# Performance work log

Hardware: AMD Instinct MI355X
Metric: run time of the kernel (lower is better)

Reference implementation:

```python
import jax, jax.numpy as jnp
import numpy as np

D_MODEL, N_HEADS, D_FF = 512, 8, 2048
B, L = 2, 2048


def layer_norm(x, g, b, eps=1e-5):
    mu = jnp.mean(x, axis=-1, keepdims=True)
    var = jnp.mean(jnp.square(x - mu), axis=-1, keepdims=True)
    return (x - mu) * jax.lax.rsqrt(var + eps) * g + b


def setup_inputs() -> dict:
    key = jax.random.key(0)
    ks = jax.random.split(key, 16)
    s = 1.0 / np.sqrt(D_MODEL)
    sf = 1.0 / np.sqrt(D_FF)
    return {
        "x": jax.random.normal(ks[0], (B, L, D_MODEL), jnp.float32),
        "Wq": jax.random.normal(ks[1], (D_MODEL, D_MODEL), jnp.float32) * s,
        "bq": jnp.zeros((D_MODEL,), jnp.float32),
        "Wk": jax.random.normal(ks[2], (D_MODEL, D_MODEL), jnp.float32) * s,
        "bk": jnp.zeros((D_MODEL,), jnp.float32),
        "Wv": jax.random.normal(ks[3], (D_MODEL, D_MODEL), jnp.float32) * s,
        "bv": jnp.zeros((D_MODEL,), jnp.float32),
        "Wo": jax.random.normal(ks[4], (D_MODEL, D_MODEL), jnp.float32) * s,
        "bo": jnp.zeros((D_MODEL,), jnp.float32),
        "W1": jax.random.normal(ks[5], (D_FF, D_MODEL), jnp.float32) * s,   # conv1 k=1 -> linear
        "b1": jnp.zeros((D_FF,), jnp.float32),
        "W2": jax.random.normal(ks[6], (D_MODEL, D_FF), jnp.float32) * sf,  # conv2 k=1 -> linear
        "b2": jnp.zeros((D_MODEL,), jnp.float32),
        "g1": jnp.ones((D_MODEL,), jnp.float32),
        "be1": jnp.zeros((D_MODEL,), jnp.float32),
        "g2": jnp.ones((D_MODEL,), jnp.float32),
        "be2": jnp.zeros((D_MODEL,), jnp.float32),
    }


def reference(x, Wq, bq, Wk, bk, Wv, bv, Wo, bo, W1, b1, W2, b2, g1, be1, g2, be2):
    Bx, Lx, D = x.shape
    H = N_HEADS
    dk = D // H
    # projections -> [B, L, H, dk]
    q = (x @ Wq.T + bq).reshape(Bx, Lx, H, dk)
    k = (x @ Wk.T + bk).reshape(Bx, Lx, H, dk)
    v = (x @ Wv.T + bv).reshape(Bx, Lx, H, dk)
    scale = 1.0 / jnp.sqrt(jnp.asarray(dk, x.dtype))
    scores = jnp.einsum('blhd,bshd->bhls', q, k)  # full LxL score tensor (as in source)
    A = jax.nn.softmax(scale * scores, axis=-1)
    out = jnp.einsum('bhls,bshd->blhd', A, v).reshape(Bx, Lx, D)
    attn_out = out @ Wo.T + bo
    # residual + norm1 (dropout is identity in eval)
    x1 = layer_norm(x + attn_out, g1, be1)
    # FFN: conv1d with kernel_size=1 == pointwise linear
    y = jax.nn.relu(x1 @ W1.T + b1)
    y = y @ W2.T + b2
    return layer_norm(x1 + y, g2, be2)
```

## Files before the change

### kernel.cpp

```cpp
#include <hip/hip_runtime.h>
#include <hip/hip_bf16.h>
#include <cstddef>

#define SEQ 2048
#define DM  512
#define NH  8
#define DKH 64
#define DFF 2048
#define NB  2
#define MR  (NB*SEQ)

typedef __attribute__((ext_vector_type(8)))  short short8;
typedef __attribute__((ext_vector_type(4)))  float f32x4;
typedef __attribute__((ext_vector_type(16))) float f32x16;

#define AS1(p) ((const __attribute__((address_space(1))) void*)(p))
#define AS3(p) ((__attribute__((address_space(3))) void*)(p))

#define QSCALE 0.180336880f

__device__ inline unsigned cvtpk(float lo, float hi) {
  unsigned r;
  asm("v_cvt_pk_bf16_f32 %0, %1, %2" : "=v"(r) : "v"(lo), "v"(hi));
  return r;
}

__device__ inline void cvt8(const float* __restrict__ s, __hip_bfloat16* __restrict__ d) {
  float4 a = *reinterpret_cast<const float4*>(s);
  float4 b = *reinterpret_cast<const float4*>(s + 4);
  union { __hip_bfloat16 h[8]; short8 v; } u;
  u.h[0] = __float2bfloat16(a.x); u.h[1] = __float2bfloat16(a.y);
  u.h[2] = __float2bfloat16(a.z); u.h[3] = __float2bfloat16(a.w);
  u.h[4] = __float2bfloat16(b.x); u.h[5] = __float2bfloat16(b.y);
  u.h[6] = __float2bfloat16(b.z); u.h[7] = __float2bfloat16(b.w);
  *reinterpret_cast<short8*>(d) = u.v;
}

__global__ __launch_bounds__(256) void cvt_all(
    const float* __restrict__ x,
    const float* __restrict__ Wq, const float* __restrict__ Wk,
    const float* __restrict__ Wv, const float* __restrict__ Wo,
    const float* __restrict__ W1, const float* __restrict__ W2,
    const float* __restrict__ bq, const float* __restrict__ bk,
    const float* __restrict__ bv,
    __hip_bfloat16* __restrict__ xb,  __hip_bfloat16* __restrict__ wqkv,
    __hip_bfloat16* __restrict__ wob, __hip_bfloat16* __restrict__ w1b,
    __hip_bfloat16* __restrict__ w2b, float* __restrict__ bqkv)
{
  const int u = blockIdx.x * 256 + threadIdx.x;
  if (u < 262144) {
    cvt8(x + (size_t)u * 8, xb + (size_t)u * 8);
  } else if (u < 360448) {
    const int d = (u - 262144) * 8;
    const int n = d >> 9, k = d & 511;
    const float* src = (n < 512) ? (Wq + (size_t)n * 512 + k)
                     : (n < 1024) ? (Wk + (size_t)(n - 512) * 512 + k)
                                  : (Wv + (size_t)(n - 1024) * 512 + k);
    cvt8(src, wqkv + d);
  } else if (u < 393216) {
    const int d = (u - 360448) * 8; cvt8(Wo + d, wob + d);
  } else if (u < 524288) {
    const int d = (u - 393216) * 8; cvt8(W1 + d, w1b + d);
  } else if (u < 655360) {
    const int d = (u - 524288) * 8; cvt8(W2 + d, w2b + d);
  } else if (u < 655552) {
    const int d = (u - 655360) * 8;
    const float* src = (d < 512) ? (bq + d) : (d < 1024) ? (bk + d - 512) : (bv + d - 1024);
    *reinterpret_cast<float4*>(bqkv + d)     = *reinterpret_cast<const float4*>(src);
    *reinterpret_cast<float4*>(bqkv + d + 4) = *reinterpret_cast<const float4*>(src + 4);
  }
}

template<int OUT_BF16, int RELU, int WVT, int SPLITK>
__global__ __launch_bounds__(256) void gemm_bt(
    const __hip_bfloat16* __restrict__ A, const __hip_bfloat16* __restrict__ Bt,
    const float* __restrict__ bias, void* __restrict__ Cout, void* __restrict__ Cout1,
    __hip_bfloat16* __restrict__ qkbO, __hip_bfloat16* __restrict__ vtO,
    int M, int N, int K)
{
  __shared__ __align__(16) char lds[32768];
  const int t = threadIdx.x, lane = t & 63, w = t >> 6;
  const int m0 = blockIdx.y * 128, n0 = blockIdx.x * 128;
  const int wm = w >> 1, wn = w & 1;
  const int z = (SPLITK == 2) ? blockIdx.z : 0;
  const int Keff = (SPLITK == 2) ? (K >> 1) : K;
  const int koff = z * Keff;
  const int g = lane >> 4;

  const int r0   = t >> 2;
  const int kofs = ((lane & 3) ^ (r0 & 3)) * 8;
  const __hip_bfloat16* a0 = A  + (size_t)(m0 + r0)      * K + koff + kofs;
  const __hip_bfloat16* a1 = A  + (size_t)(m0 + r0 + 64) * K + koff + kofs;
  const __hip_bfloat16* b0 = Bt + (size_t)(n0 + r0)      * K + koff + kofs;
  const __hip_bfloat16* b1 = Bt + (size_t)(n0 + r0 + 64) * K + koff + kofs;
  const int ldsoff = t * 16;

  const int ca = (lane >> 4) ^ (lane & 3);
  const int fA = (wm * 64 + (lane & 15)) * 64 + ca * 16;
  const int fB = (wn * 64 + (lane & 15)) * 64 + ca * 16;

  f32x4 acc[4][4] = {};
  const int nkt = Keff >> 5;

  auto STAGE = [&](int buf, int kt) {
    const size_t ko = (size_t)kt * 32;
    char* bb = lds + buf * 16384;
    __builtin_amdgcn_global_load_lds(AS1(a0 + ko), AS3(bb + ldsoff),         16, 0, 0);
    __builtin_amdgcn_global_load_lds(AS1(a1 + ko), AS3(bb + 4096  + ldsoff), 16, 0, 0);
    __builtin_amdgcn_global_load_lds(AS1(b0 + ko), AS3(bb + 8192  + ldsoff), 16, 0, 0);
    __builtin_amdgcn_global_load_lds(AS1(b1 + ko), AS3(bb + 12288 + ldsoff), 16, 0, 0);
  };

  STAGE(0, 0);
  __syncthreads();
  int cur = 0;

  for (int kt = 0; kt < nkt; ++kt) {
    STAGE(cur ^ 1, kt + 1 < nkt ? kt + 1 : kt);
    const char* Ab = lds + cur * 16384;
    const char* Bb = Ab + 8192;
    short8 af[4], bf[4];
#pragma unroll
    for (int i = 0; i < 4; ++i) af[i] = *reinterpret_cast<const short8*>(Ab + fA + i * 1024);
#pragma unroll
    for (int j = 0; j < 4; ++j) bf[j] = *reinterpret_cast<const short8*>(Bb + fB + j * 1024);
    __builtin_amdgcn_s_setprio(1);
#pragma unroll
    for (int i = 0; i < 4; ++i)
#pragma unroll
      for (int j = 0; j < 4; ++j)
        acc[i][j] = __builtin_amdgcn_mfma_f32_16x16x32_bf16(af[i], bf[j], acc[i][j], 0, 0, 0);
    __builtin_amdgcn_s_setprio(0);
    __syncthreads();
    cur ^= 1;
  }

  float bcol[4];
#pragma unroll
  for (int j = 0; j < 4; ++j)
    bcol[j] = (SPLITK == 2 && z) ? 0.f : bias[n0 + wn * 64 + j * 16 + (lane & 15)];

  if (WVT && n0 >= 1024) {
#pragma unroll
    for (int i = 0; i < 4; ++i) {
      const int r = m0 + wm * 64 + i * 16 + (g << 2);
      const int bb = r >> 11, s = r & 2047;
#pragma unroll
      for (int j = 0; j < 4; ++j) {
        const int hd = n0 + wn * 64 + j * 16 + (lane & 15) - 1024;
        union { __hip_bfloat16 h[4]; uint2 uu; } pk;
#pragma unroll
        for (int jj = 0; jj < 4; ++jj) pk.h[jj] = __float2bfloat16(acc[i][j][jj] + bcol[j]);
        *reinterpret_cast<uint2*>(vtO + ((size_t)(bb * 8 + (hd >> 6)) * 64 + (hd & 63)) * SEQ + s) = pk.uu;
      }
    }
    return;
  }

  const float qsc = (WVT && n0 < 512) ? QSCALE : 1.0f;
#pragma unroll
  for (int i = 0; i < 4; ++i) {
    const int row = m0 + wm * 64 + i * 16 + (g << 2);
#pragma unroll
    for (int j = 0; j < 4; ++j) {
      const int col = n0 + wn * 64 + j * 16 + (lane & 15);
#pragma unroll
      for (int jj = 0; jj < 4; ++jj) {
        float v = acc[i][j][jj] + bcol[j];
        if (RELU) v = fmaxf(v, 0.f);
        if (WVT)
          qkbO[(size_t)(row + jj) * 1024 + col] = __float2bfloat16(v * qsc);
        else if (OUT_BF16)
          ((__hip_bfloat16*)Cout)[(size_t)(row + jj) * N + col] = __float2bfloat16(v);
        else {
          float* dst = (float*)((SPLITK == 2 && z) ? Cout1 : Cout);
          dst[(size_t)(row + jj) * N + col] = v;
        }
      }
    }
  }
}

__global__ __launch_bounds__(256) void attn_mfma(
    const __hip_bfloat16* __restrict__ qkb, const __hip_bfloat16* __restrict__ vtb,
    __hip_bfloat16* __restrict__ po, float* __restrict__ pm, float* __restrict__ pl)
{
  __shared__ __align__(16) char lds[32768];
  char* ks = lds;
  char* vT = lds + 16384;

  const int t = threadIdx.x, lane = t & 63, w = t >> 6;
  const int qt = blockIdx.x, bh = blockIdx.y, z = blockIdx.z;
  const int b = bh >> 3, h = bh & 7;
  const int ST0 = z * (SEQ / 4);
  const int NT = SEQ / 4 / 64;
  const int l31 = lane & 31, hi = lane >> 5;
  const int swz = (lane & 7) << 4;
  const int hi16 = hi * 16;

  const __hip_bfloat16* Qg = qkb + (size_t)b * SEQ * 1024 + h * DKH;
  const int qrow = qt * 128 + w * 32 + l31;
  short8 qf[4];
#pragma unroll
  for (int kc = 0; kc < 4; ++kc)
    qf[kc] = *reinterpret_cast<const short8*>(Qg + (size_t)qrow * 1024 + kc * 16 + hi * 8);

  const int srow = t >> 3;
  const int sofs = ((lane & 7) ^ (srow & 7)) * 8;
  const __hip_bfloat16* kbase = qkb + (size_t)(b * SEQ + ST0 + srow) * 1024 + 512 + h * DKH + sofs;
  const __hip_bfloat16* vbase = vtb + ((size_t)bh * 64 + srow) * SEQ + ST0 + sofs;
  const int ldso = t * 16;

  f32x16 o0 = {}, o1 = {};
  float m_ = -1e30f, l_ = 0.f;

  auto STAGE_K = [&](int buf, int st) {
    const size_t ko = (size_t)st * 64 * 1024;
    char* kd = ks + buf * 8192 + ldso;
    __builtin_amdgcn_global_load_lds(AS1(kbase + ko),                     AS3(kd),        16, 0, 0);
    __builtin_amdgcn_global_load_lds(AS1(kbase + ko + (size_t)32 * 1024), AS3(kd + 4096), 16, 0, 0);
  };
  auto STAGE_V = [&](int buf, int st) {
    const size_t vo = (size_t)st * 64;
    char* vd = vT + buf * 8192 + ldso;
    __builtin_amdgcn_global_load_lds(AS1(vbase + vo),                    AS3(vd),        16, 0, 0);
    __builtin_amdgcn_global_load_lds(AS1(vbase + vo + (size_t)32 * SEQ), AS3(vd + 4096), 16, 0, 0);
  };

  STAGE_K(0, 0);
  STAGE_V(0, 0);
  __syncthreads();
  int cur = 0;

  for (int st = 0; st < NT; ++st) {
    const int nxt = st + 1 < NT ? st + 1 : st;
    STAGE_V(cur ^ 1, nxt);
    STAGE_K(cur ^ 1, nxt);
    const char* kb_ = ks + cur * 8192;
    const char* vb_ = vT + cur * 8192;

#pragma unroll
    for (int half = 0; half < 2; ++half) {
      const int rbase = (half * 32 + l31) * 128;

      f32x16 acc = {};
      __builtin_amdgcn_s_setprio(1);
#pragma unroll
      for (int kc = 0; kc < 4; ++kc) {
        const int kbyte = (kc * 32 + hi16) ^ swz;
        const short8 ka = *reinterpret_cast<const short8*>(kb_ + rbase + kbyte);
        acc = __builtin_amdgcn_mfma_f32_32x32x16_bf16(ka, qf[kc], acc, 0, 0, 0);
      }
      __builtin_amdgcn_s_setprio(0);

      float tm[8];
#pragma unroll
      for (int r = 0; r < 8; ++r) tm[r] = fmaxf(acc[r], acc[r + 8]);
#pragma unroll
      for (int sft = 4; sft >= 1; sft >>= 1)
#pragma unroll
        for (int r = 0; r < sft; ++r) tm[r] = fmaxf(tm[r], tm[r + sft]);
      float pmax = fmaxf(tm[0], __shfl_xor(tm[0], 32));

      const bool skip = __all(pmax <= m_ + 8.0f);
      float al = 1.0f;
      if (!skip) {
        const float mn = fmaxf(m_, pmax);
        al = exp2f(m_ - mn);
        m_ = mn;
      }

      short8 pf[2];
      float ps = 0.f;
#pragma unroll
      for (int sc = 0; sc < 2; ++sc) {
        const int rb = sc * 8;
        float e0 = exp2f(acc[rb+0] - m_), e1 = exp2f(acc[rb+1] - m_);
        float e2 = exp2f(acc[rb+2] - m_), e3 = exp2f(acc[rb+3] - m_);
        float e4 = exp2f(acc[rb+4] - m_), e5 = exp2f(acc[rb+5] - m_);
        float e6 = exp2f(acc[rb+6] - m_), e7 = exp2f(acc[rb+7] - m_);
        ps += ((e0 + e1) + (e2 + e3)) + ((e4 + e5) + (e6 + e7));
        unsigned w0 = cvtpk(e0, e1), w1 = cvtpk(e2, e3);
        unsigned w2 = cvtpk(e4, e5), w3 = cvtpk(e6, e7);
        asm("v_permlane32_swap_b32 %0, %1" : "+v"(w0), "+v"(w2));
        asm("v_permlane32_swap_b32 %0, %1" : "+v"(w1), "+v"(w3));
        union { unsigned u[4]; short8 s8; } pu;
        pu.u[0] = w0; pu.u[1] = w1; pu.u[2] = w2; pu.u[3] = w3;
        pf[sc] = pu.s8;
      }
      ps += __shfl_xor(ps, 32);
      l_ = l_ * al + ps;
      if (!skip) {
#pragma unroll
        for (int r = 0; r < 16; ++r) { o0[r] *= al; o1[r] *= al; }
      }

      __builtin_amdgcn_s_setprio(1);
#pragma unroll
      for (int kc = 0; kc < 2; ++kc) {
        const int sbyte = (half * 64 + kc * 32 + hi16) ^ swz;
        const short8 va0 = *reinterpret_cast<const short8*>(vb_ + l31 * 128 + sbyte);
        const short8 va1 = *reinterpret_cast<const short8*>(vb_ + (32 + l31) * 128 + sbyte);
        o0 = __builtin_amdgcn_mfma_f32_32x32x16_bf16(va0, pf[kc], o0, 0, 0, 0);
        o1 = __builtin_amdgcn_mfma_f32_32x32x16_bf16(va1, pf[kc], o1, 0, 0, 0);
      }
      __builtin_amdgcn_s_setprio(0);
    }

    __syncthreads();
    cur ^= 1;
  }

  {
    __hip_bfloat16* pz = po + (size_t)z * MR * DM;
    const size_t orow = (size_t)b * SEQ + qt * 128 + w * 32 + l31;
    __hip_bfloat16* dst = pz + orow * DM + h * DKH;
#pragma unroll
    for (int r = 0; r < 4; ++r) {
      uint2 u0, u1;
      u0.x = cvtpk(o0[4*r+0], o0[4*r+1]); u0.y = cvtpk(o0[4*r+2], o0[4*r+3]);
      u1.x = cvtpk(o1[4*r+0], o1[4*r+1]); u1.y = cvtpk(o1[4*r+2], o1[4*r+3]);
      *reinterpret_cast<uint2*>(dst + r * 8 + hi * 4)      = u0;
      *reinterpret_cast<uint2*>(dst + 32 + r * 8 + hi * 4) = u1;
    }
  }
  if (lane < 32) {
    const size_t idx = ((size_t)z * 16 + bh) * SEQ + qt * 128 + w * 32 + lane;
    pm[idx] = m_;
    pl[idx] = l_;
  }
}

__global__ __launch_bounds__(256) void attn_combine(
    const __hip_bfloat16* __restrict__ po, const float* __restrict__ pm,
    const float* __restrict__ pl, __hip_bfloat16* __restrict__ attnb)
{
  const int row  = blockIdx.x * 4 + (threadIdx.x >> 6);
  const int lane = threadIdx.x & 63;
  const int d0 = lane * 8, h = lane >> 3;
  const int b = row >> 11, qq = row & 2047;
  const size_t idx = ((size_t)b * 8 + h) * SEQ + qq;
  const size_t zs = (size_t)16 * SEQ;
  const float m0 = pm[idx], m1 = pm[idx + zs], m2 = pm[idx + 2*zs], m3 = pm[idx + 3*zs];
  const float l0 = pl[idx], l1 = pl[idx + zs], l2 = pl[idx + 2*zs], l3 = pl[idx + 3*zs];
  const float M = fmaxf(fmaxf(m0, m1), fmaxf(m2, m3));
  const float a0 = exp2f(m0 - M), a1 = exp2f(m1 - M);
  const float a2 = exp2f(m2 - M), a3 = exp2f(m3 - M);
  const float inv = 1.0f / (l0*a0 + l1*a1 + l2*a2 + l3*a3);
  float az[4] = {a0, a1, a2, a3};
  float acc[8] = {};
  const size_t ro = (size_t)row * DM + d0;
#pragma unroll
  for (int zz = 0; zz < 4; ++zz) {
    short8 v = *reinterpret_cast<const short8*>(po + (size_t)zz * MR * DM + ro);
#pragma unroll
    for (int j = 0; j < 8; ++j) {
      const unsigned uu = ((unsigned)(unsigned short)v[j]) << 16;
      acc[j] += az[zz] * __builtin_bit_cast(float, uu);
    }
  }
  union { __hip_bfloat16 hh[8]; short8 s8; } u;
#pragma unroll
  for (int j = 0; j < 8; ++j) u.hh[j] = __float2bfloat16(acc[j] * inv);
  *reinterpret_cast<short8*>(attnb + ro) = u.s8;
}

template<int WB>
__global__ __launch_bounds__(256) void ln_res(
    const float* __restrict__ X, const float* __restrict__ Y0,
    const float* __restrict__ Y1,
    const float* __restrict__ g, const float* __restrict__ be,
    float* __restrict__ out, __hip_bfloat16* __restrict__ outb)
{
  const int row  = blockIdx.x * 4 + (threadIdx.x >> 6);
  const int lane = threadIdx.x & 63;
  const int c0   = lane * 8;
  const float* xr = X  + (size_t)row * DM;
  const float* y0 = Y0 + (size_t)row * DM;
  const float* y1 = Y1 + (size_t)row * DM;

  float v[8];
  float4 a0 = *reinterpret_cast<const float4*>(xr + c0);
  float4 a1 = *reinterpret_cast<const float4*>(xr + c0 + 4);
  float4 b0 = *reinterpret_cast<const float4*>(y0 + c0);
  float4 b1 = *reinterpret_cast<const float4*>(y0 + c0 + 4);
  float4 c0v= *reinterpret_cast<const float4*>(y1 + c0);
  float4 c1v= *reinterpret_cast<const float4*>(y1 + c0 + 4);
  v[0]=a0.x+b0.x+c0v.x; v[1]=a0.y+b0.y+c0v.y; v[2]=a0.z+b0.z+c0v.z; v[3]=a0.w+b0.w+c0v.w;
  v[4]=a1.x+b1.x+c1v.x; v[5]=a1.y+b1.y+c1v.y; v[6]=a1.z+b1.z+c1v.z; v[7]=a1.w+b1.w+c1v.w;

  float s = 0.f;
#pragma unroll
  for (int i = 0; i < 8; ++i) s += v[i];
#pragma unroll
  for (int off = 32; off >= 1; off >>= 1) s += __shfl_xor(s, off);
  const float mu = s * (1.0f/512.0f);

  float ss = 0.f;
#pragma unroll
  for (int i = 0; i < 8; ++i) { const float d = v[i] - mu; ss += d*d; }
#pragma unroll
  for (int off = 32; off >= 1; off >>= 1) ss += __shfl_xor(ss, off);
  const float rs = rsqrtf(ss * (1.0f/512.0f) + 1e-5f);

  float4 g0 = *reinterpret_cast<const float4*>(g  + c0);
  float4 g1 = *reinterpret_cast<const float4*>(g  + c0 + 4);
  float4 e0 = *reinterpret_cast<const float4*>(be + c0);
  float4 e1 = *reinterpret_cast<const float4*>(be + c0 + 4);
  float r[8];
  r[0]=(v[0]-mu)*rs*g0.x+e0.x; r[1]=(v[1]-mu)*rs*g0.y+e0.y;
  r[2]=(v[2]-mu)*rs*g0.z+e0.z; r[3]=(v[3]-mu)*rs*g0.w+e0.w;
  r[4]=(v[4]-mu)*rs*g1.x+e1.x; r[5]=(v[5]-mu)*rs*g1.y+e1.y;
  r[6]=(v[6]-mu)*rs*g1.z+e1.z; r[7]=(v[7]-mu)*rs*g1.w+e1.w;
  float4 o0, o1;
  o0.x=r[0]; o0.y=r[1]; o0.z=r[2]; o0.w=r[3];
  o1.x=r[4]; o1.y=r[5]; o1.z=r[6]; o1.w=r[7];
  *reinterpret_cast<float4*>(out + (size_t)row * DM + c0)     = o0;
  *reinterpret_cast<float4*>(out + (size_t)row * DM + c0 + 4) = o1;
  if (WB) {
    union { __hip_bfloat16 h[8]; short8 vv; } u;
#pragma unroll
    for (int i = 0; i < 8; ++i) u.h[i] = __float2bfloat16(r[i]);
    *reinterpret_cast<short8*>(outb + (size_t)row * DM + c0) = u.vv;
  }
}

extern "C" void kernel_launch(void* const* d_in, const int* in_sizes, int n_in,
                              void* d_out, int out_size, void* d_ws, size_t ws_size,
                              hipStream_t stream)
{
  const float* x   = (const float*)d_in[0];
  const float* Wq  = (const float*)d_in[1];
  const float* bq  = (const float*)d_in[2];
  const float* Wk  = (const float*)d_in[3];
  const float* bk  = (const float*)d_in[4];
  const float* Wv  = (const float*)d_in[5];
  const float* bv  = (const float*)d_in[6];
  const float* Wo  = (const float*)d_in[7];
  const float* bo  = (const float*)d_in[8];
  const float* W1  = (const float*)d_in[9];
  const float* b1  = (const float*)d_in[10];
  const float* W2  = (const float*)d_in[11];
  const float* b2  = (const float*)d_in[12];
  const float* g1  = (const float*)d_in[13];
  const float* be1 = (const float*)d_in[14];
  const float* g2  = (const float*)d_in[15];
  const float* be2 = (const float*)d_in[16];
  float* out = (float*)d_out;

  char* p = (char*)d_ws;
  __hip_bfloat16* xb    = (__hip_bfloat16*)p;  p += 4194304;
  __hip_bfloat16* wqkv  = (__hip_bfloat16*)p;  p += 1572864;
  __hip_bfloat16* wob   = (__hip_bfloat16*)p;  p += 524288;
  __hip_bfloat16* w1b   = (__hip_bfloat16*)p;  p += 2097152;
  __hip_bfloat16* w2b   = (__hip_bfloat16*)p;  p += 2097152;
  float*          bqkv  = (float*)p;           p += 8192;
  __hip_bfloat16* qkb   = (__hip_bfloat16*)p;  p += 8388608;
  __hip_bfloat16* vtb   = (__hip_bfloat16*)p;  p += 4194304;
  __hip_bfloat16* pob   = (__hip_bfloat16*)p;  p += 16777216;
  float*          pm    = (float*)p;           p += 524288;
  float*          pl    = (float*)p;           p += 524288;
  float*          oproj = (float*)p;           p += 8388608;
  __hip_bfloat16* x1b   = (__hip_bfloat16*)p;  p += 4194304;

  float*          x1    = (float*)qkb;
  __hip_bfloat16* attnb = (__hip_bfloat16*)vtb;
  float*          opa   = (float*)pob;
  __hip_bfloat16* f1b   = pob;
  float*          y2a   = (float*)d_ws;
  float*          y2b   = oproj;

  const dim3 blk(256);

  cvt_all<<<dim3(2561), blk, 0, stream>>>(x, Wq, Wk, Wv, Wo, W1, W2, bq, bk, bv,
                                          xb, wqkv, wob, w1b, w2b, bqkv);
  gemm_bt<1,0,1,0><<<dim3(12, 32), blk, 0, stream>>>(xb, wqkv, bqkv, nullptr, nullptr, qkb, vtb, MR, 1536, DM);
  attn_mfma   <<<dim3(SEQ/128, NB*NH, 4), blk, 0, stream>>>(qkb, vtb, pob, pm, pl);
  attn_combine<<<dim3(MR/4), blk, 0, stream>>>(pob, pm, pl, attnb);
  gemm_bt<0,0,0,2><<<dim3(4, 32, 2), blk, 0, stream>>>(attnb, wob, bo, opa, oproj, nullptr, nullptr, MR, DM, DM);
  ln_res<1><<<dim3(MR/4), blk, 0, stream>>>(x, opa, oproj, g1, be1, x1, x1b);
  gemm_bt<1,1,0,0><<<dim3(16, 32), blk, 0, stream>>>(x1b, w1b, b1, f1b, nullptr, nullptr, nullptr, MR, DFF, DM);
  gemm_bt<0,0,0,2><<<dim3(4, 32, 2), blk, 0, stream>>>(f1b, w2b, b2, y2a, y2b, nullptr, nullptr, MR, DM, DFF);
  ln_res<0><<<dim3(MR/4), blk, 0, stream>>>(x1, y2a, y2b, g2, be2, out, nullptr);
}
```

Before: 133.3 us.

## Double GEMM K-tile depth to 64 and unroll double-buffered loops by two

The GEMM kernel now stages 64-wide K tiles (64KB LDS, 8-way XOR swizzle) instead of 32-wide, halving the number of barriers per K and doing two MFMA sub-steps per stage. Both the GEMM and attention main loops are manually unrolled by two with fixed buffer addresses, removing runtime buffer-index arithmetic. The larger LDS footprint may reduce occupancy for the GEMM blocks. The attention loop assumes an even tile count.

```diff
diff --git a/kernel.cpp b/kernel.cpp
--- a/kernel.cpp
+++ b/kernel.cpp
@@ -78,7 +78,7 @@
     __hip_bfloat16* __restrict__ qkbO, __hip_bfloat16* __restrict__ vtO,
     int M, int N, int K)
 {
-  __shared__ __align__(16) char lds[32768];
+  __shared__ __align__(16) char lds[65536];
   const int t = threadIdx.x, lane = t & 63, w = t >> 6;
   const int m0 = blockIdx.y * 128, n0 = blockIdx.x * 128;
   const int wm = w >> 1, wn = w & 1;
@@ -87,52 +87,58 @@
   const int koff = z * Keff;
   const int g = lane >> 4;
 
-  const int r0   = t >> 2;
-  const int kofs = ((lane & 3) ^ (r0 & 3)) * 8;
-  const __hip_bfloat16* a0 = A  + (size_t)(m0 + r0)      * K + koff + kofs;
-  const __hip_bfloat16* a1 = A  + (size_t)(m0 + r0 + 64) * K + koff + kofs;
-  const __hip_bfloat16* b0 = Bt + (size_t)(n0 + r0)      * K + koff + kofs;
-  const __hip_bfloat16* b1 = Bt + (size_t)(n0 + r0 + 64) * K + koff + kofs;
+  const int r0   = t >> 3;
+  const int kofs = ((lane & 7) ^ (r0 & 7)) * 8;
+  const __hip_bfloat16* ap = A  + (size_t)(m0 + r0) * K + koff + kofs;
+  const __hip_bfloat16* bp = Bt + (size_t)(n0 + r0) * K + koff + kofs;
   const int ldsoff = t * 16;
 
-  const int ca = (lane >> 4) ^ (lane & 3);
-  const int fA = (wm * 64 + (lane & 15)) * 64 + ca * 16;
-  const int fB = (wn * 64 + (lane & 15)) * 64 + ca * 16;
+  const int fA = (wm * 64 + (lane & 15)) * 128;
+  const int fB = (wn * 64 + (lane & 15)) * 128;
+  const int sw = lane & 7;
 
   f32x4 acc[4][4] = {};
-  const int nkt = Keff >> 5;
+  const int nkt = Keff >> 6;
 
   auto STAGE = [&](int buf, int kt) {
-    const size_t ko = (size_t)kt * 32;
-    char* bb = lds + buf * 16384;
-    __builtin_amdgcn_global_load_lds(AS1(a0 + ko), AS3(bb + ldsoff),         16, 0, 0);
-    __builtin_amdgcn_global_load_lds(AS1(a1 + ko), AS3(bb + 4096  + ldsoff), 16, 0, 0);
-    __builtin_amdgcn_global_load_lds(AS1(b0 + ko), AS3(bb + 8192  + ldsoff), 16, 0, 0);
-    __builtin_amdgcn_global_load_lds(AS1(b1 + ko), AS3(bb + 12288 + ldsoff), 16, 0, 0);
+    const size_t ko = (size_t)kt * 64;
+    char* bb = lds + buf * 32768;
+#pragma unroll
+    for (int ii = 0; ii < 4; ++ii) {
+      __builtin_amdgcn_global_load_lds(AS1(ap + (size_t)ii * 32 * K + ko), AS3(bb + ii * 4096 + ldsoff),         16, 0, 0);
+      __builtin_amdgcn_global_load_lds(AS1(bp + (size_t)ii * 32 * K + ko), AS3(bb + 16384 + ii * 4096 + ldsoff), 16, 0, 0);
+    }
+  };
+  auto COMPUTE = [&](const char* bb) {
+    const char* Ab = bb;
+    const char* Bb = bb + 16384;
+#pragma unroll
+    for (int kk = 0; kk < 2; ++kk) {
+      const int cx = ((kk * 4 + g) ^ sw) * 16;
+      short8 af[4], bf[4];
+#pragma unroll
+      for (int i = 0; i < 4; ++i) af[i] = *reinterpret_cast<const short8*>(Ab + fA + i * 2048 + cx);
+#pragma unroll
+      for (int j = 0; j < 4; ++j) bf[j] = *reinterpret_cast<const short8*>(Bb + fB + j * 2048 + cx);
+      __builtin_amdgcn_s_setprio(1);
+#pragma unroll
+      for (int i = 0; i < 4; ++i)
+#pragma unroll
+        for (int j = 0; j < 4; ++j)
+          acc[i][j] = __builtin_amdgcn_mfma_f32_16x16x32_bf16(af[i], bf[j], acc[i][j], 0, 0, 0);
+      __builtin_amdgcn_s_setprio(0);
+    }
   };
 
   STAGE(0, 0);
   __syncthreads();
-  int cur = 0;
-
-  for (int kt = 0; kt < nkt; ++kt) {
-    STAGE(cur ^ 1, kt + 1 < nkt ? kt + 1 : kt);
-    const char* Ab = lds + cur * 16384;
-    const char* Bb = Ab + 8192;
-    short8 af[4], bf[4];
-#pragma unroll
-    for (int i = 0; i < 4; ++i) af[i] = *reinterpret_cast<const short8*>(Ab + fA + i * 1024);
-#pragma unroll
-    for (int j = 0; j < 4; ++j) bf[j] = *reinterpret_cast<const short8*>(Bb + fB + j * 1024);
-    __builtin_amdgcn_s_setprio(1);
-#pragma unroll
-    for (int i = 0; i < 4; ++i)
-#pragma unroll
-      for (int j = 0; j < 4; ++j)
-        acc[i][j] = __builtin_amdgcn_mfma_f32_16x16x32_bf16(af[i], bf[j], acc[i][j], 0, 0, 0);
-    __builtin_amdgcn_s_setprio(0);
+  for (int kt = 0; kt < nkt; kt += 2) {
+    STAGE(1, kt + 1 < nkt ? kt + 1 : kt);
+    COMPUTE(lds);
     __syncthreads();
-    cur ^= 1;
+    STAGE(0, kt + 2 < nkt ? kt + 2 : kt);
+    COMPUTE(lds + 32768);
+    __syncthreads();
   }
 
   float bcol[4];
@@ -227,18 +233,7 @@
     __builtin_amdgcn_global_load_lds(AS1(vbase + vo + (size_t)32 * SEQ), AS3(vd + 4096), 16, 0, 0);
   };
 
-  STAGE_K(0, 0);
-  STAGE_V(0, 0);
-  __syncthreads();
-  int cur = 0;
-
-  for (int st = 0; st < NT; ++st) {
-    const int nxt = st + 1 < NT ? st + 1 : st;
-    STAGE_V(cur ^ 1, nxt);
-    STAGE_K(cur ^ 1, nxt);
-    const char* kb_ = ks + cur * 8192;
-    const char* vb_ = vT + cur * 8192;
-
+  auto TILE = [&](const char* kb_, const char* vb_) {
 #pragma unroll
     for (int half = 0; half < 2; ++half) {
       const int rbase = (half * 32 + l31) * 128;
@@ -306,9 +301,22 @@
       }
       __builtin_amdgcn_s_setprio(0);
     }
-
+  };
+
+  STAGE_K(0, 0);
+  STAGE_V(0, 0);
+  __syncthreads();
+
+  for (int st = 0; st < NT; st += 2) {
+    STAGE_V(1, st + 1);
+    STAGE_K(1, st + 1);
+    TILE(ks, vT);
     __syncthreads();
-    cur ^= 1;
+    const int nx = st + 2 < NT ? st + 2 : st + 1;
+    STAGE_V(0, nx);
+    STAGE_K(0, nx);
+    TILE(ks + 8192, vT + 8192);
+    __syncthreads();
   }
 
   {
```

After: 122.5 us. 1.09x faster.
